# Performance work log

Measured on AMD Instinct MI355X. Metric: run time of the kernel, lower is better.

## Reference

```python
import jax, jax.numpy as jnp
import numpy as np

N_NODES = 50000
N_EDGES = 1600000
IN_DIM = 128
HEADS = 4
HID = 16
NEG_SLOPE = 0.2  # DGL GATConv default


def setup_inputs() -> dict:
    key = jax.random.key(0)
    ks = jax.random.split(key, 7)
    features = jax.random.normal(ks[0], (N_NODES, IN_DIM), dtype=jnp.float32)
    W = jax.random.normal(ks[1], (IN_DIM, HEADS * HID), dtype=jnp.float32) * 0.1
    attn_l = jax.random.normal(ks[2], (HEADS, HID), dtype=jnp.float32) * 0.1
    attn_r = jax.random.normal(ks[3], (HEADS, HID), dtype=jnp.float32) * 0.1
    bias = jax.random.normal(ks[4], (HEADS * HID,), dtype=jnp.float32) * 0.1
    src = jax.random.randint(ks[5], (N_EDGES,), 0, N_NODES, dtype=jnp.int64)
    dst = jax.random.randint(ks[6], (N_EDGES,), 0, N_NODES, dtype=jnp.int64)
    return {"features": features, "W": W, "attn_l": attn_l, "attn_r": attn_r,
            "bias": bias, "src": src, "dst": dst}


def reference(features, W, attn_l, attn_r, bias, src, dst):
    N = features.shape[0]
    H, D = attn_l.shape
    # linear projection -> per-head features [N, H, D]
    feat = (features @ W).reshape(N, H, D)
    el = jnp.einsum('nhd,hd->nh', feat, attn_l)  # [N, H]
    er = jnp.einsum('nhd,hd->nh', feat, attn_r)  # [N, H]
    # per-edge unnormalized attention logits [E, H]
    e = jax.nn.leaky_relu(el[src] + er[dst], negative_slope=NEG_SLOPE)
    # edge softmax segmented by destination node (numerically stable)
    emax = jax.ops.segment_max(e, dst, num_segments=N)
    ee = jnp.exp(e - emax[dst])
    denom = jax.ops.segment_sum(ee, dst, num_segments=N)
    alpha = ee / denom[dst]  # [E, H]
    # weighted neighbor aggregation: scatter-add of alpha * feat[src]
    msg = feat[src] * alpha[:, :, None]  # [E, H, D]
    out = jax.ops.segment_sum(msg, dst, num_segments=N)  # [N, H, D]
    out = out + bias.reshape(1, H, D)
    # wrapper GAT.forward averages over heads
    return out.mean(axis=1)  # [N, D]
```

## Files before the change

kernel.cpp:

```cpp
#include <hip/hip_runtime.h>
#include <hip/hip_bf16.h>

#define IN_DIM 128
#define HEADS 4
#define HID 16
#define HD 64
#define NEG_SLOPE 0.2f
#define PSHIFT 7
#define PCAP 5120
#define NPMAX 512
#define EPB 8192
#define NB_PROJ 256
#define NTILE 5

typedef __attribute__((ext_vector_type(8))) short bf16x8;
typedef __attribute__((ext_vector_type(4))) float f32x4;

__device__ __forceinline__ float lrelu_exp(float x) {
    float e = x > 0.0f ? x : NEG_SLOPE * x;
    return __expf(e);
}

__device__ __forceinline__ unsigned short f2bf(float x) {
    unsigned int u = __float_as_uint(x);
    return (unsigned short)((u + 0x7fffu + ((u >> 16) & 1u)) >> 16);
}

__global__ __launch_bounds__(256) void k_prjpart(const float* __restrict__ features,
                                                 const float* __restrict__ W,
                                                 const float* __restrict__ attn_l,
                                                 const float* __restrict__ attn_r,
                                                 __hip_bfloat16* __restrict__ feat16,
                                                 float* __restrict__ el,
                                                 float* __restrict__ er,
                                                 const int* __restrict__ src,
                                                 const int* __restrict__ dst,
                                                 int* __restrict__ cursor,
                                                 unsigned int* __restrict__ partbuf,
                                                 int n_nodes, int n_edges,
                                                 int npart, int npartblk) {
    __shared__ float smem[IN_DIM * HD];

    if (blockIdx.x < (unsigned)npartblk) {
        int* hist = (int*)smem;
        int* base = (int*)smem + NPMAX;
        const int t = threadIdx.x;
        for (int i = t; i < npart; i += 256) hist[i] = 0;
        __syncthreads();

        const int e0 = blockIdx.x * EPB;
        unsigned int vals[32];
#pragma unroll
        for (int j = 0; j < 8; ++j) {
            int e = e0 + j * 1024 + t * 4;
            if (e + 4 <= n_edges) {
                int4 s4 = *reinterpret_cast<const int4*>(src + e);
                int4 d4 = *reinterpret_cast<const int4*>(dst + e);
                vals[j * 4 + 0] = ((unsigned)d4.x << 16) | (unsigned)s4.x;
                vals[j * 4 + 1] = ((unsigned)d4.y << 16) | (unsigned)s4.y;
                vals[j * 4 + 2] = ((unsigned)d4.z << 16) | (unsigned)s4.z;
                vals[j * 4 + 3] = ((unsigned)d4.w << 16) | (unsigned)s4.w;
            } else {
#pragma unroll
                for (int k = 0; k < 4; ++k) {
                    int ee = e + k;
                    vals[j * 4 + k] = (ee < n_edges)
                        ? (((unsigned)dst[ee] << 16) | (unsigned)src[ee])
                        : 0xffffffffu;
                }
            }
        }
#pragma unroll
        for (int j = 0; j < 32; ++j)
            if (vals[j] != 0xffffffffu) atomicAdd(&hist[vals[j] >> (16 + PSHIFT)], 1);
        __syncthreads();
        for (int i = t; i < npart; i += 256) {
            base[i] = atomicAdd(&cursor[i], hist[i]);
            hist[i] = 0;
        }
        __syncthreads();
#pragma unroll
        for (int j = 0; j < 32; ++j) {
            unsigned int v = vals[j];
            if (v != 0xffffffffu) {
                int p = v >> (16 + PSHIFT);
                int idx = base[p] + atomicAdd(&hist[p], 1);
                if (idx < PCAP) partbuf[(size_t)p * PCAP + idx] = v;
            }
        }
        return;
    }

    for (int i = threadIdx.x; i < IN_DIM * HD; i += 256) smem[i] = W[i];
    __syncthreads();

    uint4 ent[NTILE];
#pragma unroll
    for (int i = 0; i < NTILE; ++i) {
        const int e  = threadIdx.x + (i << 8);
        const int fi = e >> 6;
        const int ln = e & 63;
        const int c  = fi >> 2;
        const int q  = fi & 3;
        const int colid = ln & 15;
        const int quad  = ln >> 4;
        unsigned short v[8];
        if (c < 4) {
#pragma unroll
            for (int j = 0; j < 8; ++j) {
                int k = q * 32 + quad * 8 + j;
                v[j] = f2bf(smem[k * HD + c * 16 + colid]);
            }
        } else if (colid < 8) {
            const int h = colid & 3;
            const float* attn = (colid < 4) ? attn_l : attn_r;
            float at[16];
#pragma unroll
            for (int d = 0; d < 16; ++d) at[d] = attn[h * 16 + d];
#pragma unroll
            for (int j = 0; j < 8; ++j) {
                int k = q * 32 + quad * 8 + j;
                float sum = 0.f;
#pragma unroll
                for (int d = 0; d < 16; ++d)
                    sum = fmaf(smem[k * HD + h * 16 + d], at[d], sum);
                v[j] = f2bf(sum);
            }
        } else {
#pragma unroll
            for (int j = 0; j < 8; ++j) v[j] = 0;
        }
        ent[i].x = (unsigned int)v[0] | ((unsigned int)v[1] << 16);
        ent[i].y = (unsigned int)v[2] | ((unsigned int)v[3] << 16);
        ent[i].z = (unsigned int)v[4] | ((unsigned int)v[5] << 16);
        ent[i].w = (unsigned int)v[6] | ((unsigned int)v[7] << 16);
    }
    __syncthreads();

    uint4* fragw = (uint4*)smem;
#pragma unroll
    for (int i = 0; i < NTILE; ++i)
        fragw[threadIdx.x + (i << 8)] = ent[i];
    __syncthreads();

    const bf16x8* frags = (const bf16x8*)smem;
    const int lane  = threadIdx.x & 63;
    const int wave  = threadIdx.x >> 6;
    const int colid = lane & 15;
    const int quad  = lane >> 4;

    const int ngroups = (n_nodes + 15) >> 4;
    const int gwave = (blockIdx.x - npartblk) * 4 + wave;
    const int nwaves = NB_PROJ * 4;

    int g = gwave;
    float4 ra[8];
    if (g < ngroups) {
        int rown = g * 16 + colid;
        if (rown >= n_nodes) rown = n_nodes - 1;
        const float* fp = features + (size_t)rown * IN_DIM + quad * 8;
#pragma unroll
        for (int q = 0; q < 4; ++q) {
            ra[q * 2]     = *reinterpret_cast<const float4*>(fp + q * 32);
            ra[q * 2 + 1] = *reinterpret_cast<const float4*>(fp + q * 32 + 4);
        }
    }

    while (g < ngroups) {
        const int gn = g + nwaves;
        float4 rb[8];
        if (gn < ngroups) {
            int rown = gn * 16 + colid;
            if (rown >= n_nodes) rown = n_nodes - 1;
            const float* fp = features + (size_t)rown * IN_DIM + quad * 8;
#pragma unroll
            for (int q = 0; q < 4; ++q) {
                rb[q * 2]     = *reinterpret_cast<const float4*>(fp + q * 32);
                rb[q * 2 + 1] = *reinterpret_cast<const float4*>(fp + q * 32 + 4);
            }
        }

        const int n0 = g * 16;
        f32x4 acc[NTILE];
#pragma unroll
        for (int c = 0; c < NTILE; ++c) acc[c] = (f32x4){0.f, 0.f, 0.f, 0.f};

#pragma unroll
        for (int q = 0; q < 4; ++q) {
            float4 a0 = ra[q * 2];
            float4 a1 = ra[q * 2 + 1];
            bf16x8 av;
            av[0] = (short)f2bf(a0.x); av[1] = (short)f2bf(a0.y);
            av[2] = (short)f2bf(a0.z); av[3] = (short)f2bf(a0.w);
            av[4] = (short)f2bf(a1.x); av[5] = (short)f2bf(a1.y);
            av[6] = (short)f2bf(a1.z); av[7] = (short)f2bf(a1.w);
#pragma unroll
            for (int c = 0; c < NTILE; ++c) {
                bf16x8 bv = frags[(c * 4 + q) * 64 + lane];
                acc[c] = __builtin_amdgcn_mfma_f32_16x16x32_bf16(av, bv, acc[c], 0, 0, 0);
            }
        }

        const bool full = (n0 + 16 <= n_nodes);
#pragma unroll
        for (int c = 0; c < 4; ++c) {
#pragma unroll
            for (int r = 0; r < 4; ++r) {
                int n = n0 + quad * 4 + r;
                if (full || n < n_nodes) {
                    ((unsigned short*)feat16)[(size_t)n * HD + c * 16 + colid] = f2bf(acc[c][r]);
                }
            }
        }
        if (colid < 8) {
            float* dstp = (colid < 4) ? el : er;
            const int h = colid & 3;
#pragma unroll
            for (int r = 0; r < 4; ++r) {
                int n = n0 + quad * 4 + r;
                if (full || n < n_nodes) {
                    dstp[(size_t)n * HEADS + h] = acc[4][r];
                }
            }
        }

#pragma unroll
        for (int j = 0; j < 8; ++j) ra[j] = rb[j];
        g = gn;
    }
}

__global__ __launch_bounds__(512) void k_sort(const unsigned int* __restrict__ partbuf,
                                              const int* __restrict__ cursor,
                                              unsigned short* __restrict__ csr,
                                              int* __restrict__ row_ptr,
                                              unsigned short* __restrict__ deg16,
                                              int n_nodes) {
    __shared__ int hist[128];
    __shared__ int scan_s[128];
    const int p = blockIdx.x;
    const int t = threadIdx.x;
    const int count = min(cursor[p], PCAP);
    const unsigned int* buf = partbuf + (size_t)p * PCAP;

    unsigned int vals[10];
#pragma unroll
    for (int j = 0; j < 10; ++j) {
        int i = t + j * 512;
        vals[j] = (i < count) ? buf[i] : 0xffffffffu;
    }

    if (t < 128) hist[t] = 0;
    __syncthreads();
#pragma unroll
    for (int j = 0; j < 10; ++j)
        if (vals[j] != 0xffffffffu) atomicAdd(&hist[(vals[j] >> 16) & 127], 1);
    __syncthreads();

    int v = 0;
    if (t < 128) {
        v = hist[t];
        scan_s[t] = v;
    }
    __syncthreads();
    for (int off = 1; off < 128; off <<= 1) {
        int u = (t >= off && t < 128) ? scan_s[t - off] : 0;
        __syncthreads();
        if (t < 128) scan_s[t] += u;
        __syncthreads();
    }
    if (t < 128) {
        const int excl = scan_s[t] - v;
        const int node = (p << PSHIFT) + t;
        if (node < n_nodes) {
            row_ptr[node] = p * PCAP + excl;
            deg16[node] = (unsigned short)v;
        }
        hist[t] = excl;
    }
    __syncthreads();
    unsigned short* cbase = csr + (size_t)p * PCAP;
#pragma unroll
    for (int j = 0; j < 10; ++j) {
        unsigned int val = vals[j];
        if (val != 0xffffffffu) {
            int ld = (val >> 16) & 127;
            int pos = atomicAdd(&hist[ld], 1);
            cbase[pos] = (unsigned short)(val & 0xffffu);
        }
    }
}

__global__ __launch_bounds__(256) void k_agg(const int* __restrict__ row_ptr,
                                             const unsigned short* __restrict__ deg16,
                                             const unsigned short* __restrict__ csr,
                                             const float* __restrict__ el,
                                             const float* __restrict__ er,
                                             const unsigned int* __restrict__ feat16u,
                                             const float* __restrict__ bias,
                                             float* __restrict__ out,
                                             int n_nodes) {
    int n = (blockIdx.x * blockDim.x + threadIdx.x) >> 6;
    if (n >= n_nodes) return;
    const int lane = threadIdx.x & 63;
    const int eW = lane >> 2;
    const int hW = lane & 3;
    const int slot = lane & 15;
    const int h2 = slot >> 2;
    const int dq = slot & 3;
    const int egrp = lane >> 4;
    const int foff = slot << 1;

    const int beg = row_ptr[n];
    const int deg = (int)deg16[n];
    const unsigned short* row = csr + beg;
    const float erW = er[(size_t)n * HEADS + hW];

    float aA0 = 0.f, aA1 = 0.f, aA2 = 0.f, aA3 = 0.f;
    float aB0 = 0.f, aB1 = 0.f, aB2 = 0.f, aB3 = 0.f;
    float denacc = 0.f;

    bool valid = (eW < deg);
    int s = valid ? (int)row[eW] : 0;
    float w = valid ? lrelu_exp(el[(size_t)s * HEADS + hW] + erW) : 0.f;

    for (int i0 = 0; i0 < deg; i0 += 16) {
        denacc += w;
        const unsigned int pw = ((unsigned int)f2bf(w) << 16) | (unsigned int)s;

        unsigned int pk[4];
#pragma unroll
        for (int r = 0; r < 4; ++r)
            pk[r] = __shfl(pw, ((((r << 2) | egrp) << 2) | h2));

        const bool v2 = (i0 + 16 + eW < deg);
        int s2 = v2 ? (int)row[i0 + 16 + eW] : 0;

        uint2 pf[4];
#pragma unroll
        for (int r = 0; r < 4; ++r) {
            pf[r] = make_uint2(0u, 0u);
            if (i0 + (r << 2) < deg)
                pf[r] = *reinterpret_cast<const uint2*>(
                    feat16u + (((size_t)(pk[r] & 0xffffu)) << 5) + foff);
        }

        float w2 = v2 ? lrelu_exp(el[(size_t)s2 * HEADS + hW] + erW) : 0.f;

#pragma unroll
        for (int r = 0; r < 4; ++r) {
            float wj = __uint_as_float(pk[r] & 0xffff0000u);
            float x0 = __uint_as_float(pf[r].x << 16);
            float x1 = __uint_as_float(pf[r].x & 0xffff0000u);
            float x2 = __uint_as_float(pf[r].y << 16);
            float x3 = __uint_as_float(pf[r].y & 0xffff0000u);
            if (r & 1) {
                aB0 = fmaf(wj, x0, aB0); aB1 = fmaf(wj, x1, aB1);
                aB2 = fmaf(wj, x2, aB2); aB3 = fmaf(wj, x3, aB3);
            } else {
                aA0 = fmaf(wj, x0, aA0); aA1 = fmaf(wj, x1, aA1);
                aA2 = fmaf(wj, x2, aA2); aA3 = fmaf(wj, x3, aA3);
            }
        }
        s = s2;
        w = w2;
    }

    float den = denacc;
    den += __shfl_xor(den, 4);
    den += __shfl_xor(den, 8);
    den += __shfl_xor(den, 16);
    den += __shfl_xor(den, 32);
    float denh = __shfl(den, h2);
    float inv = (denh > 0.f) ? 0.25f / denh : 0.f;

    float r0 = (aA0 + aB0) * inv;
    float r1 = (aA1 + aB1) * inv;
    float r2 = (aA2 + aB2) * inv;
    float r3 = (aA3 + aB3) * inv;
#pragma unroll
    for (int m = 4; m <= 32; m <<= 1) {
        r0 += __shfl_xor(r0, m);
        r1 += __shfl_xor(r1, m);
        r2 += __shfl_xor(r2, m);
        r3 += __shfl_xor(r3, m);
    }
    if (lane < 4) {
        const int d0 = lane * 4;
        float4 o;
        o.x = r0 + 0.25f * (bias[d0]     + bias[16 + d0]     + bias[32 + d0]     + bias[48 + d0]);
        o.y = r1 + 0.25f * (bias[d0 + 1] + bias[16 + d0 + 1] + bias[32 + d0 + 1] + bias[48 + d0 + 1]);
        o.z = r2 + 0.25f * (bias[d0 + 2] + bias[16 + d0 + 2] + bias[32 + d0 + 2] + bias[48 + d0 + 2]);
        o.w = r3 + 0.25f * (bias[d0 + 3] + bias[16 + d0 + 3] + bias[32 + d0 + 3] + bias[48 + d0 + 3]);
        *reinterpret_cast<float4*>(out + (size_t)n * HID + d0) = o;
    }
}

extern "C" void kernel_launch(void* const* d_in, const int* in_sizes, int n_in,
                              void* d_out, int out_size, void* d_ws, size_t ws_size,
                              hipStream_t stream) {
    const float* features = (const float*)d_in[0];
    const float* W        = (const float*)d_in[1];
    const float* attn_l   = (const float*)d_in[2];
    const float* attn_r   = (const float*)d_in[3];
    const float* bias     = (const float*)d_in[4];
    const int*   src      = (const int*)d_in[5];
    const int*   dst      = (const int*)d_in[6];
    float* out = (float*)d_out;

    const int n_nodes = in_sizes[0] / IN_DIM;
    const int n_edges = in_sizes[5];
    const int npart = (n_nodes + (1 << PSHIFT) - 1) >> PSHIFT;
    const int npartblk = (n_edges + EPB - 1) / EPB;

    char* ws = (char*)d_ws;
    __hip_bfloat16* feat16 = (__hip_bfloat16*)ws; ws += (size_t)n_nodes * HD * sizeof(__hip_bfloat16);
    float* el      = (float*)ws;                  ws += (size_t)n_nodes * HEADS * sizeof(float);
    float* er      = (float*)ws;                  ws += (size_t)n_nodes * HEADS * sizeof(float);
    unsigned int* partbuf = (unsigned int*)ws;    ws += (size_t)npart * PCAP * sizeof(unsigned int);
    unsigned short* csr = (unsigned short*)ws;    ws += (size_t)npart * PCAP * sizeof(unsigned short);
    int* row_ptr   = (int*)ws;                    ws += (size_t)n_nodes * sizeof(int);
    unsigned short* deg16 = (unsigned short*)ws;  ws += (size_t)n_nodes * sizeof(unsigned short);
    int* cursor    = (int*)ws;                    ws += NPMAX * sizeof(int);

    hipMemsetAsync(cursor, 0, NPMAX * sizeof(int), stream);

    k_prjpart<<<npartblk + NB_PROJ, 256, 0, stream>>>(features, W, attn_l, attn_r,
                                                      feat16, el, er, src, dst,
                                                      cursor, partbuf,
                                                      n_nodes, n_edges, npart, npartblk);
    k_sort<<<npart, 512, 0, stream>>>(partbuf, cursor, csr, row_ptr, deg16, n_nodes);
    k_agg<<<(n_nodes + 3) / 4, 256, 0, stream>>>(row_ptr, deg16, csr, el, er,
                                                 (const unsigned int*)feat16, bias, out, n_nodes);
}
```

Baseline: 153.3 us.

## Replace partition-bucket sort with global degree count, scan, and atomic scatter

Drops the two-level partition-buffer counting sort and builds the CSR differently. A fused kernel first counts per-node in-degrees with global atomics, then a per-partition scan computes row pointers and cursors, and a scatter kernel places source ids using one global atomic per edge. This removes the intermediate partbuf write and reread and the per-partition local sort, but it adds a kernel launch, a larger memset, and 3.2M random global atomics instead of LDS atomics. Edge order within each row is now nondeterministic.

```diff
diff --git a/kernel.cpp b/kernel.cpp
--- a/kernel.cpp
+++ b/kernel.cpp
@@ -8,8 +8,7 @@
 #define NEG_SLOPE 0.2f
 #define PSHIFT 7
 #define PCAP 5120
-#define NPMAX 512
-#define EPB 8192
+#define NB_DEG 64
 #define NB_PROJ 256
 #define NTILE 5
 
@@ -26,68 +25,32 @@
     return (unsigned short)((u + 0x7fffu + ((u >> 16) & 1u)) >> 16);
 }
 
-__global__ __launch_bounds__(256) void k_prjpart(const float* __restrict__ features,
-                                                 const float* __restrict__ W,
-                                                 const float* __restrict__ attn_l,
-                                                 const float* __restrict__ attn_r,
-                                                 __hip_bfloat16* __restrict__ feat16,
-                                                 float* __restrict__ el,
-                                                 float* __restrict__ er,
-                                                 const int* __restrict__ src,
-                                                 const int* __restrict__ dst,
-                                                 int* __restrict__ cursor,
-                                                 unsigned int* __restrict__ partbuf,
-                                                 int n_nodes, int n_edges,
-                                                 int npart, int npartblk) {
+__global__ __launch_bounds__(256) void k_prjdeg(const float* __restrict__ features,
+                                                const float* __restrict__ W,
+                                                const float* __restrict__ attn_l,
+                                                const float* __restrict__ attn_r,
+                                                __hip_bfloat16* __restrict__ feat16,
+                                                float* __restrict__ el,
+                                                float* __restrict__ er,
+                                                const int* __restrict__ dst,
+                                                int* __restrict__ deg,
+                                                int n_nodes, int n_edges) {
     __shared__ float smem[IN_DIM * HD];
 
-    if (blockIdx.x < (unsigned)npartblk) {
-        int* hist = (int*)smem;
-        int* base = (int*)smem + NPMAX;
-        const int t = threadIdx.x;
-        for (int i = t; i < npart; i += 256) hist[i] = 0;
-        __syncthreads();
-
-        const int e0 = blockIdx.x * EPB;
-        unsigned int vals[32];
-#pragma unroll
-        for (int j = 0; j < 8; ++j) {
-            int e = e0 + j * 1024 + t * 4;
-            if (e + 4 <= n_edges) {
-                int4 s4 = *reinterpret_cast<const int4*>(src + e);
-                int4 d4 = *reinterpret_cast<const int4*>(dst + e);
-                vals[j * 4 + 0] = ((unsigned)d4.x << 16) | (unsigned)s4.x;
-                vals[j * 4 + 1] = ((unsigned)d4.y << 16) | (unsigned)s4.y;
-                vals[j * 4 + 2] = ((unsigned)d4.z << 16) | (unsigned)s4.z;
-                vals[j * 4 + 3] = ((unsigned)d4.w << 16) | (unsigned)s4.w;
-            } else {
-#pragma unroll
-                for (int k = 0; k < 4; ++k) {
-                    int ee = e + k;
-                    vals[j * 4 + k] = (ee < n_edges)
-                        ? (((unsigned)dst[ee] << 16) | (unsigned)src[ee])
-                        : 0xffffffffu;
-                }
-            }
-        }
-#pragma unroll
-        for (int j = 0; j < 32; ++j)
-            if (vals[j] != 0xffffffffu) atomicAdd(&hist[vals[j] >> (16 + PSHIFT)], 1);
-        __syncthreads();
-        for (int i = t; i < npart; i += 256) {
-            base[i] = atomicAdd(&cursor[i], hist[i]);
-            hist[i] = 0;
-        }
-        __syncthreads();
-#pragma unroll
-        for (int j = 0; j < 32; ++j) {
-            unsigned int v = vals[j];
-            if (v != 0xffffffffu) {
-                int p = v >> (16 + PSHIFT);
-                int idx = base[p] + atomicAdd(&hist[p], 1);
-                if (idx < PCAP) partbuf[(size_t)p * PCAP + idx] = v;
-            }
-        }
+    if (blockIdx.x < (unsigned)NB_DEG) {
+        const int t = blockIdx.x * 256 + threadIdx.x;
+        const int stride = NB_DEG * 256;
+        const int nq = n_edges >> 2;
+        const int4* dst4 = reinterpret_cast<const int4*>(dst);
+        for (int i = t; i < nq; i += stride) {
+            int4 d4 = dst4[i];
+            atomicAdd(&deg[d4.x], 1);
+            atomicAdd(&deg[d4.y], 1);
+            atomicAdd(&deg[d4.z], 1);
+            atomicAdd(&deg[d4.w], 1);
+        }
+        for (int e = (nq << 2) + t; e < n_edges; e += stride)
+            atomicAdd(&deg[dst[e]], 1);
         return;
     }
 
@@ -150,7 +113,7 @@
     const int quad  = lane >> 4;
 
     const int ngroups = (n_nodes + 15) >> 4;
-    const int gwave = (blockIdx.x - npartblk) * 4 + wave;
+    const int gwave = (blockIdx.x - NB_DEG) * 4 + wave;
     const int nwaves = NB_PROJ * 4;
 
     int g = gwave;
@@ -230,64 +193,58 @@
     }
 }
 
-__global__ __launch_bounds__(512) void k_sort(const unsigned int* __restrict__ partbuf,
-                                              const int* __restrict__ cursor,
-                                              unsigned short* __restrict__ csr,
+__global__ __launch_bounds__(128) void k_scan(const int* __restrict__ deg,
                                               int* __restrict__ row_ptr,
                                               unsigned short* __restrict__ deg16,
+                                              int* __restrict__ cur,
                                               int n_nodes) {
-    __shared__ int hist[128];
-    __shared__ int scan_s[128];
+    __shared__ int s[128];
     const int p = blockIdx.x;
     const int t = threadIdx.x;
-    const int count = min(cursor[p], PCAP);
-    const unsigned int* buf = partbuf + (size_t)p * PCAP;
-
-    unsigned int vals[10];
-#pragma unroll
-    for (int j = 0; j < 10; ++j) {
-        int i = t + j * 512;
-        vals[j] = (i < count) ? buf[i] : 0xffffffffu;
-    }
-
-    if (t < 128) hist[t] = 0;
-    __syncthreads();
-#pragma unroll
-    for (int j = 0; j < 10; ++j)
-        if (vals[j] != 0xffffffffu) atomicAdd(&hist[(vals[j] >> 16) & 127], 1);
-    __syncthreads();
-
-    int v = 0;
-    if (t < 128) {
-        v = hist[t];
-        scan_s[t] = v;
-    }
+    const int node = (p << PSHIFT) + t;
+    const int d = (node < n_nodes) ? deg[node] : 0;
+    s[t] = d;
     __syncthreads();
     for (int off = 1; off < 128; off <<= 1) {
-        int u = (t >= off && t < 128) ? scan_s[t - off] : 0;
+        int u = (t >= off) ? s[t - off] : 0;
         __syncthreads();
-        if (t < 128) scan_s[t] += u;
+        s[t] += u;
         __syncthreads();
     }
-    if (t < 128) {
-        const int excl = scan_s[t] - v;
-        const int node = (p << PSHIFT) + t;
-        if (node < n_nodes) {
-            row_ptr[node] = p * PCAP + excl;
-            deg16[node] = (unsigned short)v;
-        }
-        hist[t] = excl;
-    }
-    __syncthreads();
-    unsigned short* cbase = csr + (size_t)p * PCAP;
-#pragma unroll
-    for (int j = 0; j < 10; ++j) {
-        unsigned int val = vals[j];
-        if (val != 0xffffffffu) {
-            int ld = (val >> 16) & 127;
-            int pos = atomicAdd(&hist[ld], 1);
-            cbase[pos] = (unsigned short)(val & 0xffffu);
-        }
+    if (node < n_nodes) {
+        const int rp = p * PCAP + (s[t] - d);
+        row_ptr[node] = rp;
+        deg16[node] = (unsigned short)d;
+        cur[node] = rp;
+    }
+}
+
+__global__ __launch_bounds__(256) void k_scatter(const int* __restrict__ src,
+                                                 const int* __restrict__ dst,
+                                                 int* __restrict__ cur,
+                                                 unsigned short* __restrict__ csr,
+                                                 int n_edges) {
+    const int i = blockIdx.x * 256 + threadIdx.x;
+    const int nq = n_edges >> 2;
+    if (i < nq) {
+        const int4 s4 = reinterpret_cast<const int4*>(src)[i];
+        const int4 d4 = reinterpret_cast<const int4*>(dst)[i];
+        int pos, pb;
+        pos = atomicAdd(&cur[d4.x], 1); pb = (d4.x >> PSHIFT) * PCAP;
+        if (pos < pb + PCAP) csr[pos] = (unsigned short)s4.x;
+        pos = atomicAdd(&cur[d4.y], 1); pb = (d4.y >> PSHIFT) * PCAP;
+        if (pos < pb + PCAP) csr[pos] = (unsigned short)s4.y;
+        pos = atomicAdd(&cur[d4.z], 1); pb = (d4.z >> PSHIFT) * PCAP;
+        if (pos < pb + PCAP) csr[pos] = (unsigned short)s4.z;
+        pos = atomicAdd(&cur[d4.w], 1); pb = (d4.w >> PSHIFT) * PCAP;
+        if (pos < pb + PCAP) csr[pos] = (unsigned short)s4.w;
+    }
+    const int total = gridDim.x * 256;
+    for (int e = (nq << 2) + i; e < n_edges; e += total) {
+        const int d = dst[e];
+        const int pos = atomicAdd(&cur[d], 1);
+        const int pb = (d >> PSHIFT) * PCAP;
+        if (pos < pb + PCAP) csr[pos] = (unsigned short)src[e];
     }
 }
 
@@ -307,7 +264,6 @@
     const int hW = lane & 3;
     const int slot = lane & 15;
     const int h2 = slot >> 2;
-    const int dq = slot & 3;
     const int egrp = lane >> 4;
     const int foff = slot << 1;
 
@@ -411,25 +367,29 @@
     const int n_nodes = in_sizes[0] / IN_DIM;
     const int n_edges = in_sizes[5];
     const int npart = (n_nodes + (1 << PSHIFT) - 1) >> PSHIFT;
-    const int npartblk = (n_edges + EPB - 1) / EPB;
-
+
+    auto align16 = [](size_t x) { return (x + 15) & ~(size_t)15; };
     char* ws = (char*)d_ws;
-    __hip_bfloat16* feat16 = (__hip_bfloat16*)ws; ws += (size_t)n_nodes * HD * sizeof(__hip_bfloat16);
-    float* el      = (float*)ws;                  ws += (size_t)n_nodes * HEADS * sizeof(float);
-    float* er      = (float*)ws;                  ws += (size_t)n_nodes * HEADS * sizeof(float);
-    unsigned int* partbuf = (unsigned int*)ws;    ws += (size_t)npart * PCAP * sizeof(unsigned int);
-    unsigned short* csr = (unsigned short*)ws;    ws += (size_t)npart * PCAP * sizeof(unsigned short);
-    int* row_ptr   = (int*)ws;                    ws += (size_t)n_nodes * sizeof(int);
-    unsigned short* deg16 = (unsigned short*)ws;  ws += (size_t)n_nodes * sizeof(unsigned short);
-    int* cursor    = (int*)ws;                    ws += NPMAX * sizeof(int);
-
-    hipMemsetAsync(cursor, 0, NPMAX * sizeof(int), stream);
-
-    k_prjpart<<<npartblk + NB_PROJ, 256, 0, stream>>>(features, W, attn_l, attn_r,
-                                                      feat16, el, er, src, dst,
-                                                      cursor, partbuf,
-                                                      n_nodes, n_edges, npart, npartblk);
-    k_sort<<<npart, 512, 0, stream>>>(partbuf, cursor, csr, row_ptr, deg16, n_nodes);
+    __hip_bfloat16* feat16 = (__hip_bfloat16*)ws; ws += align16((size_t)n_nodes * HD * sizeof(__hip_bfloat16));
+    float* el      = (float*)ws;                  ws += align16((size_t)n_nodes * HEADS * sizeof(float));
+    float* er      = (float*)ws;                  ws += align16((size_t)n_nodes * HEADS * sizeof(float));
+    unsigned short* csr = (unsigned short*)ws;    ws += align16((size_t)npart * PCAP * sizeof(unsigned short));
+    int* row_ptr   = (int*)ws;                    ws += align16((size_t)n_nodes * sizeof(int));
+    unsigned short* deg16 = (unsigned short*)ws;  ws += align16((size_t)n_nodes * sizeof(unsigned short));
+    int* deg       = (int*)ws;                    ws += align16((size_t)n_nodes * sizeof(int));
+    int* cur       = (int*)ws;                    ws += align16((size_t)n_nodes * sizeof(int));
+
+    hipMemsetAsync(deg, 0, (size_t)n_nodes * sizeof(int), stream);
+
+    k_prjdeg<<<NB_DEG + NB_PROJ, 256, 0, stream>>>(features, W, attn_l, attn_r,
+                                                   feat16, el, er, dst, deg,
+                                                   n_nodes, n_edges);
+    k_scan<<<npart, 128, 0, stream>>>(deg, row_ptr, deg16, cur, n_nodes);
+    {
+        const int nq = n_edges >> 2;
+        const int nblk = (nq + 255) / 256 + 1;
+        k_scatter<<<nblk, 256, 0, stream>>>(src, dst, cur, csr, n_edges);
+    }
     k_agg<<<(n_nodes + 3) / 4, 256, 0, stream>>>(row_ptr, deg16, csr, el, er,
                                                  (const unsigned int*)feat16, bias, out, n_nodes);
 }
```

Measured after the change: 318.2 us. 2.08x slower.
